# Performance work log

Hardware: AMD Instinct MI355X
Metric: run time of the kernel (lower is better)

## Reference

```python
import jax, jax.numpy as jnp
import numpy as np

B, S, D_IN, D_HID, D_LAT = 64, 1024, 256, 512, 128
GRU_DIMS = [D_LAT, 256, 128]
D_OUT = 2
EPS_BN = 1e-5
EPS_LN = 1e-5


def _lin(key, out_d, in_d):
    k1, k2 = jax.random.split(key)
    s = 1.0 / np.sqrt(in_d)
    return (jax.random.uniform(k1, (out_d, in_d), jnp.float32, -s, s),
            jax.random.uniform(k2, (out_d,), jnp.float32, -s, s))


def setup_inputs() -> dict:
    key = jax.random.key(0)
    ks = jax.random.split(key, 16)
    x = jax.random.normal(ks[0], (B, S, D_IN), jnp.float32)
    eps = jax.random.normal(ks[1], (B, S, D_LAT), jnp.float32)
    W1lv, b1lv = _lin(ks[2], D_HID, D_IN)
    W2lv, b2lv = _lin(ks[3], D_LAT, D_HID)
    Wmu, bmu = _lin(ks[4], D_LAT, D_IN)
    Wdec, bdec = _lin(ks[5], D_IN, D_LAT)
    # GRU layer 0: in=128 -> hid=256; layer 1: in=256 -> hid=128
    Wih0, bih0 = _lin(ks[6], 3 * GRU_DIMS[1], GRU_DIMS[0])
    Whh0, bhh0 = _lin(ks[7], 3 * GRU_DIMS[1], GRU_DIMS[1])
    Wih1, bih1 = _lin(ks[8], 3 * GRU_DIMS[2], GRU_DIMS[1])
    Whh1, bhh1 = _lin(ks[9], 3 * GRU_DIMS[2], GRU_DIMS[2])
    fc_W, fc_b = _lin(ks[10], D_OUT, GRU_DIMS[2])
    return dict(
        x=x, eps=eps,
        W1lv=W1lv, b1lv=b1lv, W2lv=W2lv, b2lv=b2lv, Wmu=Wmu, bmu=bmu,
        bn_g=jnp.ones((D_LAT,), jnp.float32), bn_b=jnp.zeros((D_LAT,), jnp.float32),
        bn_rm=jnp.zeros((D_LAT,), jnp.float32), bn_rv=jnp.ones((D_LAT,), jnp.float32),
        Wdec=Wdec, bdec=bdec,
        Wih0=Wih0, Whh0=Whh0, bih0=bih0, bhh0=bhh0,
        Wih1=Wih1, Whh1=Whh1, bih1=bih1, bhh1=bhh1,
        ln_g0=jnp.ones((GRU_DIMS[1],), jnp.float32), ln_b0=jnp.zeros((GRU_DIMS[1],), jnp.float32),
        ln_g1=jnp.ones((GRU_DIMS[2],), jnp.float32), ln_b1=jnp.zeros((GRU_DIMS[2],), jnp.float32),
        fc_W=fc_W, fc_b=fc_b,
    )


def _gru_cell(x, h, Wih, Whh, bih, bhh):
    gi = x @ Wih.T + bih                      # [B, 3H]
    gh = h @ Whh.T + bhh
    ir, iz, inn = jnp.split(gi, 3, axis=-1)
    hr, hz, hn = jnp.split(gh, 3, axis=-1)
    r = jax.nn.sigmoid(ir + hr)
    zg = jax.nn.sigmoid(iz + hz)
    n = jnp.tanh(inn + r * hn)
    return (1.0 - zg) * n + zg * h


def _layernorm(h, g, b):
    m = jnp.mean(h, axis=-1, keepdims=True)
    v = jnp.var(h, axis=-1, keepdims=True)
    return (h - m) * jax.lax.rsqrt(v + EPS_LN) * g + b


def reference(x, eps, W1lv, b1lv, W2lv, b2lv, Wmu, bmu, bn_g, bn_b, bn_rm, bn_rv,
              Wdec, bdec, Wih0, Whh0, bih0, bhh0, Wih1, Whh1, bih1, bhh1,
              ln_g0, ln_b0, ln_g1, ln_b1, fc_W, fc_b):
    # --- Encoder ---
    xl = jnp.log(jax.nn.softplus(x))                       # [B,S,D_IN]
    h_enc = jax.nn.relu(xl @ W1lv.T + b1lv)                # [B,S,D_HID]
    logvar = h_enc @ W2lv.T + b2lv                         # [B,S,D_LAT]
    mu = xl @ Wmu.T + bmu                                  # [B,S,D_LAT]
    # BatchNorm1d over latent channel (eval mode, running stats)
    mu = (mu - bn_rm) * jax.lax.rsqrt(bn_rv + EPS_BN) * bn_g + bn_b
    mu = jnp.clip(mu, -10.0, 10.0)
    # --- Reparameterize ---
    z = mu + eps * jnp.exp(0.5 * logvar)                   # [B,S,D_LAT]
    # --- Decoder ---
    x_recon = jnp.exp(z @ Wdec.T + bdec)                   # [B,S,D_IN]
    # --- Stacked GRUCell + LayerNorm over time ---
    batch = x.shape[0]
    h0 = jnp.zeros((batch, GRU_DIMS[1]), z.dtype)
    h1 = jnp.zeros((batch, GRU_DIMS[2]), z.dtype)

    def step(carry, z_t):
        h0, h1 = carry
        h0 = _layernorm(_gru_cell(z_t, h0, Wih0, Whh0, bih0, bhh0), ln_g0, ln_b0)
        h1 = _layernorm(_gru_cell(h0, h1, Wih1, Whh1, bih1, bhh1), ln_g1, ln_b1)
        return (h0, h1), None

    (h0, h1), _ = jax.lax.scan(step, (h0, h1), jnp.swapaxes(z, 0, 1))
    # fc head (dropout is identity in eval mode); output_series=False
    v = h1 @ fc_W.T + fc_b                                 # [B, D_OUT]
    return (v, x_recon, mu, logvar)
```

## Files before the change

### kernel.cpp

```cpp
#include <hip/hip_runtime.h>
#include <cstdint>

typedef unsigned long long u64;

#define TOKENS 65536

#define WS_XL    0ULL
#define WS_HENC  67108864ULL
#define WS_GI0   0ULL
#define WS_XBUF0 201326592ULL
#define WS_XBUF1 (201326592ULL + 131072ULL)
#define WS_MUS   (201326592ULL + 196608ULL)
#define WS_MUT   (201326592ULL + 197120ULL)
#define WS_NEED  (201326592ULL + 197632ULL)

__global__ void k_prep(const float* __restrict__ bmu, const float* __restrict__ bng,
                       const float* __restrict__ bnb, const float* __restrict__ bnrm,
                       const float* __restrict__ bnrv,
                       float* __restrict__ mus, float* __restrict__ mut)
{
    int j = threadIdx.x;
    if (j < 128) {
        float s = bng[j] / sqrtf(bnrv[j] + 1e-5f);
        mus[j] = s;
        mut[j] = bmu[j] * s + bnb[j] - bnrm[j] * s;
    }
}

__global__ void k_xl(const float* __restrict__ x, float* __restrict__ xl, int n4)
{
    int i = blockIdx.x * blockDim.x + threadIdx.x;
    if (i >= n4) return;
    float4 v = ((const float4*)x)[i];
    float4 o;
    o.x = logf(v.x > 20.f ? v.x : log1pf(expf(v.x)));
    o.y = logf(v.y > 20.f ? v.y : log1pf(expf(v.y)));
    o.z = logf(v.z > 20.f ? v.z : log1pf(expf(v.z)));
    o.w = logf(v.w > 20.f ? v.w : log1pf(expf(v.w)));
    ((float4*)xl)[i] = o;
}

template<int EPI, int AZ>
__global__ __launch_bounds__(256) void k_gemm_f32(
    const float* __restrict__ A, const float* __restrict__ W,
    const float* __restrict__ svec, const float* __restrict__ tvec,
    float* __restrict__ C, int N, int K,
    const float* __restrict__ ZMU, const float* __restrict__ ZLV, const float* __restrict__ ZEP)
{
    __shared__ float As[32][132];
    __shared__ float Ws[32][132];
    const int tid = threadIdx.x;
    const int tx = tid & 15, ty = tid >> 4;
    const int m0 = blockIdx.x * 128;
    const int n0 = blockIdx.y * 128;
    float acc[8][8];
#pragma unroll
    for (int i = 0; i < 8; ++i)
#pragma unroll
        for (int j = 0; j < 8; ++j) acc[i][j] = 0.f;

    for (int k0 = 0; k0 < K; k0 += 32) {
#pragma unroll
        for (int it = 0; it < 4; ++it) {
            int id = tid + 256 * it;
            int r = id >> 3, c4 = id & 7;
            float4 av;
            if constexpr (AZ) {
                size_t idx = (size_t)(m0 + r) * K + k0 + c4 * 4;
                float4 m4 = *(const float4*)(ZMU + idx);
                float4 l4 = *(const float4*)(ZLV + idx);
                float4 e4 = *(const float4*)(ZEP + idx);
                av.x = m4.x + e4.x * expf(0.5f * l4.x);
                av.y = m4.y + e4.y * expf(0.5f * l4.y);
                av.z = m4.z + e4.z * expf(0.5f * l4.z);
                av.w = m4.w + e4.w * expf(0.5f * l4.w);
            } else {
                av = *(const float4*)(A + (size_t)(m0 + r) * K + k0 + c4 * 4);
            }
            float4 wv = *(const float4*)(W + (size_t)(n0 + r) * K + k0 + c4 * 4);
            As[c4*4+0][r] = av.x; As[c4*4+1][r] = av.y; As[c4*4+2][r] = av.z; As[c4*4+3][r] = av.w;
            Ws[c4*4+0][r] = wv.x; Ws[c4*4+1][r] = wv.y; Ws[c4*4+2][r] = wv.z; Ws[c4*4+3][r] = wv.w;
        }
        __syncthreads();
#pragma unroll
        for (int k = 0; k < 32; ++k) {
            float4 a0 = *(const float4*)&As[k][ty*8];
            float4 a1 = *(const float4*)&As[k][ty*8+4];
            float4 w0 = *(const float4*)&Ws[k][tx*8];
            float4 w1 = *(const float4*)&Ws[k][tx*8+4];
            float ar[8] = {a0.x,a0.y,a0.z,a0.w,a1.x,a1.y,a1.z,a1.w};
            float wr[8] = {w0.x,w0.y,w0.z,w0.w,w1.x,w1.y,w1.z,w1.w};
#pragma unroll
            for (int i = 0; i < 8; ++i)
#pragma unroll
                for (int j = 0; j < 8; ++j) acc[i][j] += ar[i] * wr[j];
        }
        __syncthreads();
    }
#pragma unroll
    for (int i = 0; i < 8; ++i) {
        size_t m = (size_t)m0 + ty*8 + i;
#pragma unroll
        for (int j4 = 0; j4 < 2; ++j4) {
            float o[4];
#pragma unroll
            for (int j = 0; j < 4; ++j) {
                int col = n0 + tx*8 + j4*4 + j;
                float v = acc[i][j4*4+j];
                if (svec) v *= svec[col];
                v += tvec[col];
                if constexpr (EPI == 1) v = fmaxf(v, 0.f);
                if constexpr (EPI == 2) v = fminf(fmaxf(v, -10.f), 10.f);
                if constexpr (EPI == 3) v = expf(v);
                o[j] = v;
            }
            *(float4*)(C + m * N + n0 + tx*8 + j4*4) = *(float4*)o;
        }
    }
}

__device__ __forceinline__ void tstore(u64* p, float v, unsigned tag) {
    u64 w = ((u64)tag << 32) | (u64)__builtin_bit_cast(unsigned, v);
    __hip_atomic_store(p, w, __ATOMIC_RELAXED, __HIP_MEMORY_SCOPE_AGENT);
}
__device__ __forceinline__ float tpoll(const u64* p, unsigned tag) {
    u64 w = 0; int guard = 0;
    do {
        w = __hip_atomic_load(p, __ATOMIC_RELAXED, __HIP_MEMORY_SCOPE_AGENT);
        if ((unsigned)(w >> 32) == tag) break;
        __builtin_amdgcn_s_sleep(1);
    } while (++guard < (1 << 17));
    return __builtin_bit_cast(float, (unsigned)w);
}
__device__ __forceinline__ void rbar() {
    asm volatile("s_waitcnt lgkmcnt(0)" ::: "memory");
    __builtin_amdgcn_s_barrier();
}

__global__ __launch_bounds__(256)
__attribute__((amdgpu_waves_per_eu(1, 1)))
void k_scan0(const float* gi0, const float* wh0, const float* bhh0,
             const float* lg0, const float* lb0,
             float* h0s, u64* xbuf)
{
    const int xcd  = blockIdx.x & 7;
    const int slot = blockIdx.x >> 3;
    const int b    = xcd * 8 + (slot >> 2);
    const int q    = slot & 3;
    const int tid = threadIdx.x;
    const int lane = tid & 63;
    const int wvi  = tid >> 6;

    __shared__ float s_h[256];
    __shared__ float s_g[192];
    __shared__ float s_r1[4], s_r2[4];

    int row = 0;
    if (tid < 192)
        row = (tid < 64) ? (64*q + tid)
            : (tid < 128) ? (256 + 64*q + (tid-64))
                          : (512 + 64*q + (tid-128));
    float4 wr[64];
    float bA = 0.f;
    if (tid < 192) {
        const float4* p = (const float4*)(wh0 + (size_t)row * 256);
#pragma unroll
        for (int i = 0; i < 64; ++i) wr[i] = p[i];
        bA = bhh0[row];
    }
    const float gv = lg0[tid], bv = lb0[tid];
    s_h[tid] = 0.f;
    __syncthreads();

    const float* gbase = gi0 + (size_t)b * 1024 * 768;
    float* hb = h0s + (size_t)b * 1024 * 256;
    u64* xb = xbuf + (size_t)b * 256;

    for (int t = 0; t < 1024; ++t) {
        float gr = 0.f, gz = 0.f, gn = 0.f;
        if (tid >= 192) {
            const float* gt = gbase + (size_t)t * 768;
            int u = 64*q + (tid - 192);
            gr = gt[u]; gz = gt[256 + u]; gn = gt[512 + u];
        } else {
            float a0 = bA, a1 = 0.f, a2 = 0.f, a3 = 0.f;
            const float4* H = (const float4*)s_h;
#pragma unroll
            for (int i = 0; i < 64; ++i) {
                float4 h4 = H[i];
                a0 += wr[i].x * h4.x; a1 += wr[i].y * h4.y;
                a2 += wr[i].z * h4.z; a3 += wr[i].w * h4.w;
            }
            s_g[tid] = (a0 + a1) + (a2 + a3);
        }
        rbar();
        if (tid >= 192) {
            int g = tid - 192;
            int u = 64*q + g;
            float r  = 1.f / (1.f + expf(-(gr + s_g[g])));
            float zg = 1.f / (1.f + expf(-(gz + s_g[64 + g])));
            float nn = tanhf(gn + r * s_g[128 + g]);
            float hn = (1.f - zg) * nn + zg * s_h[u];
            tstore(&xb[u], hn, (unsigned)(t + 1));
        }
        float hn = tpoll(&xb[tid], (unsigned)(t + 1));
        float sum = hn;
#pragma unroll
        for (int o = 32; o > 0; o >>= 1) sum += __shfl_xor(sum, o);
        if (lane == 0) s_r1[wvi] = sum;
        rbar();
        float m = (s_r1[0] + s_r1[1] + s_r1[2] + s_r1[3]) * (1.f / 256.f);
        float d = hn - m;
        float ss = d * d;
#pragma unroll
        for (int o = 32; o > 0; o >>= 1) ss += __shfl_xor(ss, o);
        if (lane == 0) s_r2[wvi] = ss;
        rbar();
        float va = (s_r2[0] + s_r2[1] + s_r2[2] + s_r2[3]) * (1.f / 256.f);
        float rs = 1.f / sqrtf(va + 1e-5f);
        float hl = d * rs * gv + bv;
        s_h[tid] = hl;
        if (q == 0) hb[(size_t)t * 256 + tid] = hl;
        rbar();
    }
}

__global__ __launch_bounds__(256)
__attribute__((amdgpu_waves_per_eu(1, 1)))
void k_scan1(const float* h0s, const float* wi1, const float* wh1,
             const float* bih1, const float* bhh1,
             const float* lg1, const float* lb1,
             const float* fcW, const float* fcb,
             float* vout, u64* xbuf)
{
    const int xcd  = blockIdx.x & 7;
    const int slot = blockIdx.x >> 3;
    const int b    = xcd * 8 + (slot >> 2);
    const int q    = slot & 3;
    const int tid = threadIdx.x;
    const int lane = tid & 63;
    const int wvi  = tid >> 6;

    __shared__ float s_x[2][256];
    __shared__ float s_h[128];
    __shared__ float s_g[192];
    __shared__ float s_r1[2], s_r2[2];

    float4 wr[64];
    float bB = 0.f;
    if (tid < 96) {
        int jj = tid;
        int row = (jj < 32) ? (32*q + jj) : (jj < 64) ? (128 + 32*q + (jj-32)) : (256 + 32*q + (jj-64));
        const float4* p = (const float4*)(wi1 + (size_t)row * 256);
#pragma unroll
        for (int i = 0; i < 64; ++i) wr[i] = p[i];
        bB = bih1[row];
    } else if (tid < 192) {
        int jj = tid - 96;
        int row = (jj < 32) ? (32*q + jj) : (jj < 64) ? (128 + 32*q + (jj-32)) : (256 + 32*q + (jj-64));
        const float4* p = (const float4*)(wh1 + (size_t)row * 128);
#pragma unroll
        for (int i = 0; i < 32; ++i) wr[i] = p[i];
        bB = bhh1[row];
    }
    float gv = 0.f, bv = 0.f;
    if (tid < 128) { gv = lg1[tid]; bv = lb1[tid]; s_h[tid] = 0.f; }
    const float4* xb4 = (const float4*)(h0s + (size_t)b * 1024 * 256);
    if (tid < 64) ((float4*)s_x[0])[tid] = xb4[tid];
    __syncthreads();

    u64* xb = xbuf + (size_t)b * 128;

    for (int t = 0; t < 1024; ++t) {
        const int cur = t & 1, nxt = cur ^ 1;
        float4 st0, st1;
        const bool stg = (tid >= 224) && (t + 1 < 1024);
        if (stg) {
            int k = tid - 224;
            st0 = xb4[(size_t)(t+1) * 64 + k];
            st1 = xb4[(size_t)(t+1) * 64 + k + 32];
        }
        if (tid < 96) {
            float a0 = bB, a1 = 0.f, a2 = 0.f, a3 = 0.f;
            const float4* X = (const float4*)s_x[cur];
#pragma unroll
            for (int i = 0; i < 64; ++i) {
                float4 h4 = X[i];
                a0 += wr[i].x * h4.x; a1 += wr[i].y * h4.y;
                a2 += wr[i].z * h4.z; a3 += wr[i].w * h4.w;
            }
            s_g[tid] = (a0 + a1) + (a2 + a3);
        } else if (tid < 192) {
            float a0 = bB, a1 = 0.f, a2 = 0.f, a3 = 0.f;
            const float4* Hh = (const float4*)s_h;
#pragma unroll
            for (int i = 0; i < 32; ++i) {
                float4 h4 = Hh[i];
                a0 += wr[i].x * h4.x; a1 += wr[i].y * h4.y;
                a2 += wr[i].z * h4.z; a3 += wr[i].w * h4.w;
            }
            s_g[96 + (tid - 96)] = (a0 + a1) + (a2 + a3);
        }
        rbar();
        if (tid >= 192 && tid < 224) {
            int g = tid - 192;
            int u = 32*q + g;
            float r  = 1.f / (1.f + expf(-(s_g[g]      + s_g[96 + g])));
            float zg = 1.f / (1.f + expf(-(s_g[32 + g] + s_g[128 + g])));
            float nn = tanhf(s_g[64 + g] + r * s_g[160 + g]);
            float hn = (1.f - zg) * nn + zg * s_h[u];
            tstore(&xb[u], hn, (unsigned)(t + 1));
        } else if (stg) {
            int k = tid - 224;
            ((float4*)s_x[nxt])[k]      = st0;
            ((float4*)s_x[nxt])[k + 32] = st1;
        }
        float hn = 0.f, d = 0.f;
        if (tid < 128) {
            hn = tpoll(&xb[tid], (unsigned)(t + 1));
            float sum = hn;
#pragma unroll
            for (int o = 32; o > 0; o >>= 1) sum += __shfl_xor(sum, o);
            if (lane == 0) s_r1[wvi] = sum;
        }
        rbar();
        if (tid < 128) {
            float m = (s_r1[0] + s_r1[1]) * (1.f / 128.f);
            d = hn - m;
            float ss = d * d;
#pragma unroll
            for (int o = 32; o > 0; o >>= 1) ss += __shfl_xor(ss, o);
            if (lane == 0) s_r2[wvi] = ss;
        }
        rbar();
        if (tid < 128) {
            float va = (s_r2[0] + s_r2[1]) * (1.f / 128.f);
            float rs = 1.f / sqrtf(va + 1e-5f);
            float hl = d * rs * gv + bv;
            s_h[tid] = hl;
        }
        rbar();
    }
    float p0 = 0.f, p1 = 0.f;
    if (tid < 128) {
        float hold = s_h[tid];
        p0 = fcW[tid] * hold;
        p1 = fcW[128 + tid] * hold;
#pragma unroll
        for (int o = 32; o > 0; o >>= 1) { p0 += __shfl_xor(p0, o); p1 += __shfl_xor(p1, o); }
        if (lane == 0) { s_r1[wvi] = p0; s_r2[wvi] = p1; }
    }
    __syncthreads();
    if (tid == 0 && q == 0) {
        vout[b * 2 + 0] = s_r1[0] + s_r1[1] + fcb[0];
        vout[b * 2 + 1] = s_r2[0] + s_r2[1] + fcb[1];
    }
}

extern "C" void kernel_launch(void* const* d_in, const int* in_sizes, int n_in,
                              void* d_out, int out_size, void* d_ws, size_t ws_size,
                              hipStream_t stream)
{
    const float* x     = (const float*)d_in[0];
    const float* eps   = (const float*)d_in[1];
    const float* W1lv  = (const float*)d_in[2];
    const float* b1lv  = (const float*)d_in[3];
    const float* W2lv  = (const float*)d_in[4];
    const float* b2lv  = (const float*)d_in[5];
    const float* Wmu   = (const float*)d_in[6];
    const float* bmu   = (const float*)d_in[7];
    const float* bn_g  = (const float*)d_in[8];
    const float* bn_b  = (const float*)d_in[9];
    const float* bn_rm = (const float*)d_in[10];
    const float* bn_rv = (const float*)d_in[11];
    const float* Wdec  = (const float*)d_in[12];
    const float* bdec  = (const float*)d_in[13];
    const float* Wih0  = (const float*)d_in[14];
    const float* Whh0  = (const float*)d_in[15];
    const float* bih0  = (const float*)d_in[16];
    const float* bhh0  = (const float*)d_in[17];
    const float* Wih1  = (const float*)d_in[18];
    const float* Whh1  = (const float*)d_in[19];
    const float* bih1  = (const float*)d_in[20];
    const float* bhh1  = (const float*)d_in[21];
    const float* ln_g0 = (const float*)d_in[22];
    const float* ln_b0 = (const float*)d_in[23];
    const float* ln_g1 = (const float*)d_in[24];
    const float* ln_b1 = (const float*)d_in[25];
    const float* fc_W  = (const float*)d_in[26];
    const float* fc_b  = (const float*)d_in[27];

    float* out   = (float*)d_out;
    float* v_out = out;
    float* xrec  = out + 128;
    float* mu    = out + 128 + 16777216;
    float* lv    = out + 128 + 16777216 + 8388608;
    float* H0S   = xrec;

    if (ws_size < WS_NEED) return;
    char* ws = (char*)d_ws;
    float* XL    = (float*)(ws + WS_XL);
    float* HENC  = (float*)(ws + WS_HENC);
    float* GI0   = (float*)(ws + WS_GI0);
    u64*   XBUF0 = (u64*)(ws + WS_XBUF0);
    u64*   XBUF1 = (u64*)(ws + WS_XBUF1);
    float* MUS   = (float*)(ws + WS_MUS);
    float* MUT   = (float*)(ws + WS_MUT);

    k_prep<<<1, 128, 0, stream>>>(bmu, bn_g, bn_b, bn_rm, bn_rv, MUS, MUT);
    k_xl<<<16384, 256, 0, stream>>>(x, XL, 4194304);
    k_gemm_f32<1,0><<<dim3(512, 4), 256, 0, stream>>>(XL,   W1lv, nullptr, b1lv, HENC, 512, 256, nullptr, nullptr, nullptr);
    k_gemm_f32<0,0><<<dim3(512, 1), 256, 0, stream>>>(HENC, W2lv, nullptr, b2lv, lv,   128, 512, nullptr, nullptr, nullptr);
    k_gemm_f32<2,0><<<dim3(512, 1), 256, 0, stream>>>(XL,   Wmu,  MUS,     MUT,  mu,   128, 256, nullptr, nullptr, nullptr);
    k_gemm_f32<0,1><<<dim3(512, 6), 256, 0, stream>>>(nullptr, Wih0, nullptr, bih0, GI0, 768, 128, mu, lv, eps);
    hipMemsetAsync(XBUF0, 0, 196608, stream);
    k_scan0<<<256, 256, 0, stream>>>(GI0, Whh0, bhh0, ln_g0, ln_b0, H0S, XBUF0);
    k_scan1<<<256, 256, 0, stream>>>(H0S, Wih1, Whh1, bih1, bhh1, ln_g1, ln_b1, fc_W, fc_b, v_out, XBUF1);
    k_gemm_f32<3,1><<<dim3(512, 2), 256, 0, stream>>>(nullptr, Wdec, nullptr, bdec, xrec, 256, 128, mu, lv, eps);
}
```

Baseline: 8.001 ms.

## Add fast sc0 exchange path with parity double-buffered tags and prefetch

The per-step cross-block exchange in both GRU scan kernels now writes each tagged hidden value twice: once with a plain sc0 store/load pair and once with the agent-scope atomic. Readers poll the fast copy a bounded number of times, then fall back to the atomic path for good. Exchange buffers are double-buffered by step parity, and the GI0 / h0s input loads are prefetched one step further ahead. The aim is to cut inter-block handoff latency on the sequential critical path, at the cost of extra stores and reliance on sc0 coherence behaviour across CUs on the same XCD.

After: 9.313 ms. 1.16x slower.

```diff
diff --git a/kernel.cpp b/kernel.cpp
--- a/kernel.cpp
+++ b/kernel.cpp
@@ -8,11 +8,13 @@
 #define WS_XL    0ULL
 #define WS_HENC  67108864ULL
 #define WS_GI0   0ULL
-#define WS_XBUF0 201326592ULL
-#define WS_XBUF1 (201326592ULL + 131072ULL)
-#define WS_MUS   (201326592ULL + 196608ULL)
-#define WS_MUT   (201326592ULL + 197120ULL)
-#define WS_NEED  (201326592ULL + 197632ULL)
+#define WS_SLOW0 201326592ULL
+#define WS_SLOW1 (201326592ULL + 262144ULL)
+#define WS_FAST0 (201326592ULL + 393216ULL)
+#define WS_FAST1 (201326592ULL + 655360ULL)
+#define WS_MUS   (201326592ULL + 786432ULL)
+#define WS_MUT   (201326592ULL + 786944ULL)
+#define WS_NEED  (201326592ULL + 787456ULL)
 
 __global__ void k_prep(const float* __restrict__ bmu, const float* __restrict__ bng,
                        const float* __restrict__ bnb, const float* __restrict__ bnrm,
@@ -119,14 +121,34 @@
     }
 }
 
-__device__ __forceinline__ void tstore(u64* p, float v, unsigned tag) {
-    u64 w = ((u64)tag << 32) | (u64)__builtin_bit_cast(unsigned, v);
+__device__ __forceinline__ u64 packtag(float v, unsigned tag) {
+    return ((u64)tag << 32) | (u64)__builtin_bit_cast(unsigned, v);
+}
+__device__ __forceinline__ void tstore(u64* p, u64 w) {
     __hip_atomic_store(p, w, __ATOMIC_RELAXED, __HIP_MEMORY_SCOPE_AGENT);
 }
-__device__ __forceinline__ float tpoll(const u64* p, unsigned tag) {
+__device__ __forceinline__ void fstore(u64* p, u64 w) {
+    asm volatile("global_store_dwordx2 %0, %1, off sc0" :: "v"(p), "v"(w) : "memory");
+}
+__device__ __forceinline__ u64 fload(const u64* p) {
+    u64 w;
+    asm volatile("global_load_dwordx2 %0, %1, off sc0\n\ts_waitcnt vmcnt(0)"
+                 : "=v"(w) : "v"(p) : "memory");
+    return w;
+}
+__device__ __forceinline__ float tpoll2(const u64* fast, const u64* slow,
+                                        unsigned tag, int& slowmode) {
+    if (!slowmode) {
+        for (int k = 0; k < 24; ++k) {
+            u64 w = fload(fast);
+            if ((unsigned)(w >> 32) == tag) return __builtin_bit_cast(float, (unsigned)w);
+            __builtin_amdgcn_s_sleep(1);
+        }
+        slowmode = 1;
+    }
     u64 w = 0; int guard = 0;
     do {
-        w = __hip_atomic_load(p, __ATOMIC_RELAXED, __HIP_MEMORY_SCOPE_AGENT);
+        w = __hip_atomic_load(slow, __ATOMIC_RELAXED, __HIP_MEMORY_SCOPE_AGENT);
         if ((unsigned)(w >> 32) == tag) break;
         __builtin_amdgcn_s_sleep(1);
     } while (++guard < (1 << 17));
@@ -141,7 +163,7 @@
 __attribute__((amdgpu_waves_per_eu(1, 1)))
 void k_scan0(const float* gi0, const float* wh0, const float* bhh0,
              const float* lg0, const float* lb0,
-             float* h0s, u64* xbuf)
+             float* h0s, u64* slow, u64* fast)
 {
     const int xcd  = blockIdx.x & 7;
     const int slot = blockIdx.x >> 3;
@@ -174,14 +196,25 @@
 
     const float* gbase = gi0 + (size_t)b * 1024 * 768;
     float* hb = h0s + (size_t)b * 1024 * 256;
-    u64* xb = xbuf + (size_t)b * 256;
+    u64* sb = slow + (size_t)b * 512;
+    u64* fb = fast + (size_t)b * 512;
+    int slowmode = 0;
+
+    float pgr = 0.f, pgz = 0.f, pgn = 0.f;
+    if (tid >= 192) {
+        int u = 64*q + lane;
+        pgr = gbase[u]; pgz = gbase[256 + u]; pgn = gbase[512 + u];
+    }
 
     for (int t = 0; t < 1024; ++t) {
-        float gr = 0.f, gz = 0.f, gn = 0.f;
+        const int par = t & 1;
+        float ngr = 0.f, ngz = 0.f, ngn = 0.f;
         if (tid >= 192) {
-            const float* gt = gbase + (size_t)t * 768;
-            int u = 64*q + (tid - 192);
-            gr = gt[u]; gz = gt[256 + u]; gn = gt[512 + u];
+            if (t + 1 < 1024) {
+                const float* gt = gbase + (size_t)(t+1) * 768;
+                int u = 64*q + lane;
+                ngr = gt[u]; ngz = gt[256 + u]; ngn = gt[512 + u];
+            }
         } else {
             float a0 = bA, a1 = 0.f, a2 = 0.f, a3 = 0.f;
             const float4* H = (const float4*)s_h;
@@ -195,15 +228,18 @@
         }
         rbar();
         if (tid >= 192) {
-            int g = tid - 192;
+            int g = lane;
             int u = 64*q + g;
-            float r  = 1.f / (1.f + expf(-(gr + s_g[g])));
-            float zg = 1.f / (1.f + expf(-(gz + s_g[64 + g])));
-            float nn = tanhf(gn + r * s_g[128 + g]);
+            float r  = 1.f / (1.f + expf(-(pgr + s_g[g])));
+            float zg = 1.f / (1.f + expf(-(pgz + s_g[64 + g])));
+            float nn = tanhf(pgn + r * s_g[128 + g]);
             float hn = (1.f - zg) * nn + zg * s_h[u];
-            tstore(&xb[u], hn, (unsigned)(t + 1));
-        }
-        float hn = tpoll(&xb[tid], (unsigned)(t + 1));
+            u64 w = packtag(hn, (unsigned)(t + 1));
+            fstore(&fb[par * 256 + u], w);
+            tstore(&sb[par * 256 + u], w);
+        }
+        float hn = tpoll2(&fb[par * 256 + tid], &sb[par * 256 + tid],
+                          (unsigned)(t + 1), slowmode);
         float sum = hn;
 #pragma unroll
         for (int o = 32; o > 0; o >>= 1) sum += __shfl_xor(sum, o);
@@ -222,6 +258,7 @@
         s_h[tid] = hl;
         if (q == 0) hb[(size_t)t * 256 + tid] = hl;
         rbar();
+        pgr = ngr; pgz = ngz; pgn = ngn;
     }
 }
 
@@ -231,7 +268,7 @@
              const float* bih1, const float* bhh1,
              const float* lg1, const float* lb1,
              const float* fcW, const float* fcb,
-             float* vout, u64* xbuf)
+             float* vout, u64* slow, u64* fast)
 {
     const int xcd  = blockIdx.x & 7;
     const int slot = blockIdx.x >> 3;
@@ -267,18 +304,26 @@
     if (tid < 128) { gv = lg1[tid]; bv = lb1[tid]; s_h[tid] = 0.f; }
     const float4* xb4 = (const float4*)(h0s + (size_t)b * 1024 * 256);
     if (tid < 64) ((float4*)s_x[0])[tid] = xb4[tid];
+    float4 pp0 = {0,0,0,0}, pp1 = {0,0,0,0};
+    if (tid >= 224) {
+        int k = tid - 224;
+        pp0 = xb4[(size_t)64 + k];
+        pp1 = xb4[(size_t)64 + k + 32];
+    }
     __syncthreads();
 
-    u64* xb = xbuf + (size_t)b * 128;
+    u64* sb = slow + (size_t)b * 256;
+    u64* fb = fast + (size_t)b * 256;
+    int slowmode = 0;
 
     for (int t = 0; t < 1024; ++t) {
         const int cur = t & 1, nxt = cur ^ 1;
-        float4 st0, st1;
-        const bool stg = (tid >= 224) && (t + 1 < 1024);
-        if (stg) {
+        const int par = t & 1;
+        float4 nn0 = {0,0,0,0}, nn1 = {0,0,0,0};
+        if (tid >= 224 && t + 2 < 1024) {
             int k = tid - 224;
-            st0 = xb4[(size_t)(t+1) * 64 + k];
-            st1 = xb4[(size_t)(t+1) * 64 + k + 32];
+            nn0 = xb4[(size_t)(t+2) * 64 + k];
+            nn1 = xb4[(size_t)(t+2) * 64 + k + 32];
         }
         if (tid < 96) {
             float a0 = bB, a1 = 0.f, a2 = 0.f, a3 = 0.f;
@@ -309,15 +354,18 @@
             float zg = 1.f / (1.f + expf(-(s_g[32 + g] + s_g[128 + g])));
             float nn = tanhf(s_g[64 + g] + r * s_g[160 + g]);
             float hn = (1.f - zg) * nn + zg * s_h[u];
-            tstore(&xb[u], hn, (unsigned)(t + 1));
-        } else if (stg) {
+            u64 w = packtag(hn, (unsigned)(t + 1));
+            fstore(&fb[par * 128 + u], w);
+            tstore(&sb[par * 128 + u], w);
+        } else if (tid >= 224 && t + 1 < 1024) {
             int k = tid - 224;
-            ((float4*)s_x[nxt])[k]      = st0;
-            ((float4*)s_x[nxt])[k + 32] = st1;
+            ((float4*)s_x[nxt])[k]      = pp0;
+            ((float4*)s_x[nxt])[k + 32] = pp1;
         }
         float hn = 0.f, d = 0.f;
         if (tid < 128) {
-            hn = tpoll(&xb[tid], (unsigned)(t + 1));
+            hn = tpoll2(&fb[par * 128 + tid], &sb[par * 128 + tid],
+                        (unsigned)(t + 1), slowmode);
             float sum = hn;
 #pragma unroll
             for (int o = 32; o > 0; o >>= 1) sum += __shfl_xor(sum, o);
@@ -340,6 +388,7 @@
             s_h[tid] = hl;
         }
         rbar();
+        pp0 = nn0; pp1 = nn1;
     }
     float p0 = 0.f, p1 = 0.f;
     if (tid < 128) {
@@ -402,8 +451,10 @@
     float* XL    = (float*)(ws + WS_XL);
     float* HENC  = (float*)(ws + WS_HENC);
     float* GI0   = (float*)(ws + WS_GI0);
-    u64*   XBUF0 = (u64*)(ws + WS_XBUF0);
-    u64*   XBUF1 = (u64*)(ws + WS_XBUF1);
+    u64*   SLOW0 = (u64*)(ws + WS_SLOW0);
+    u64*   SLOW1 = (u64*)(ws + WS_SLOW1);
+    u64*   FAST0 = (u64*)(ws + WS_FAST0);
+    u64*   FAST1 = (u64*)(ws + WS_FAST1);
     float* MUS   = (float*)(ws + WS_MUS);
     float* MUT   = (float*)(ws + WS_MUT);
 
@@ -413,8 +464,8 @@
     k_gemm_f32<0,0><<<dim3(512, 1), 256, 0, stream>>>(HENC, W2lv, nullptr, b2lv, lv,   128, 512, nullptr, nullptr, nullptr);
     k_gemm_f32<2,0><<<dim3(512, 1), 256, 0, stream>>>(XL,   Wmu,  MUS,     MUT,  mu,   128, 256, nullptr, nullptr, nullptr);
     k_gemm_f32<0,1><<<dim3(512, 6), 256, 0, stream>>>(nullptr, Wih0, nullptr, bih0, GI0, 768, 128, mu, lv, eps);
-    hipMemsetAsync(XBUF0, 0, 196608, stream);
-    k_scan0<<<256, 256, 0, stream>>>(GI0, Whh0, bhh0, ln_g0, ln_b0, H0S, XBUF0);
-    k_scan1<<<256, 256, 0, stream>>>(H0S, Wih1, Whh1, bih1, bhh1, ln_g1, ln_b1, fc_W, fc_b, v_out, XBUF1);
+    hipMemsetAsync(SLOW0, 0, 786432, stream);
+    k_scan0<<<256, 256, 0, stream>>>(GI0, Whh0, bhh0, ln_g0, ln_b0, H0S, SLOW0, FAST0);
+    k_scan1<<<256, 256, 0, stream>>>(H0S, Wih1, Whh1, bih1, bhh1, ln_g1, ln_b1, fc_W, fc_b, v_out, SLOW1, FAST1);
     k_gemm_f32<3,1><<<dim3(512, 2), 256, 0, stream>>>(nullptr, Wdec, nullptr, bdec, xrec, 256, 128, mu, lv, eps);
 }
```

## Hoist GRU layer-1 input projection out of scan and drop cross-block polling

Applied to the files above, without the earlier changes.

The layer-1 input-gate projection (h0 @ Wih1) moves out of the sequential scan into a separate parallel kernel that writes gi1 to the workspace. The layer-1 scan then runs one 512-thread block per batch row, holding only the Whh1 rows in registers and prefetching gi1 two steps ahead. This removes the per-step global store/poll exchange between four blocks and shortens the serial critical path. The cost is an extra ~100MB workspace round-trip and only 64 active blocks during the scan.

After: 6.906 ms (median of 2 runs). 13.7% less time.

```diff
diff --git a/kernel.cpp b/kernel.cpp
--- a/kernel.cpp
+++ b/kernel.cpp
@@ -8,8 +8,8 @@
 #define WS_XL    0ULL
 #define WS_HENC  67108864ULL
 #define WS_GI0   0ULL
+#define WS_GI1   0ULL
 #define WS_XBUF0 201326592ULL
-#define WS_XBUF1 (201326592ULL + 131072ULL)
 #define WS_MUS   (201326592ULL + 196608ULL)
 #define WS_MUT   (201326592ULL + 197120ULL)
 #define WS_NEED  (201326592ULL + 197632ULL)
@@ -227,70 +227,109 @@
 
 __global__ __launch_bounds__(256)
 __attribute__((amdgpu_waves_per_eu(1, 1)))
-void k_scan1(const float* h0s, const float* wi1, const float* wh1,
-             const float* bih1, const float* bhh1,
-             const float* lg1, const float* lb1,
-             const float* fcW, const float* fcb,
-             float* vout, u64* xbuf)
-{
-    const int xcd  = blockIdx.x & 7;
-    const int slot = blockIdx.x >> 3;
-    const int b    = xcd * 8 + (slot >> 2);
-    const int q    = slot & 3;
+void k_gi1(const float* h0s, const float* wi1, const float* bih1, float* gi1)
+{
+    const int bx = blockIdx.x;
+    const int by = blockIdx.y;
+    const int tid = threadIdx.x;
+    __shared__ float s_x[2][4][256];
+
+    float4 wr[64];
+    float bB = 0.f;
+    const int row = by * 192 + tid;
+    if (tid < 192) {
+        const float4* p = (const float4*)(wi1 + (size_t)row * 256);
+#pragma unroll
+        for (int i = 0; i < 64; ++i) wr[i] = p[i];
+        bB = bih1[row];
+    }
+    const float4* xb4 = (const float4*)(h0s + (size_t)bx * 256 * 256);
+    if (tid >= 192) {
+        int s = tid - 192;
+#pragma unroll
+        for (int j = 0; j < 4; ++j)
+            ((float4*)s_x[0][j])[s] = xb4[(size_t)j * 64 + s];
+    }
+    __syncthreads();
+    for (int r = 0; r < 64; ++r) {
+        const int cur = r & 1;
+        float4 pf[4];
+        const bool stg = (tid >= 192) && (r + 1 < 64);
+        if (stg) {
+            int s = tid - 192;
+#pragma unroll
+            for (int j = 0; j < 4; ++j)
+                pf[j] = xb4[(size_t)((r + 1) * 4 + j) * 64 + s];
+        }
+        if (tid < 192) {
+#pragma unroll 1
+            for (int j = 0; j < 4; ++j) {
+                float a0 = bB, a1 = 0.f, a2 = 0.f, a3 = 0.f;
+                const float4* X = (const float4*)s_x[cur][j];
+#pragma unroll
+                for (int i = 0; i < 64; ++i) {
+                    float4 h4 = X[i];
+                    a0 += wr[i].x * h4.x; a1 += wr[i].y * h4.y;
+                    a2 += wr[i].z * h4.z; a3 += wr[i].w * h4.w;
+                }
+                gi1[(size_t)(bx * 256 + r * 4 + j) * 384 + row] = (a0 + a1) + (a2 + a3);
+            }
+        } else if (stg) {
+            int s = tid - 192;
+#pragma unroll
+            for (int j = 0; j < 4; ++j)
+                ((float4*)s_x[cur ^ 1][j])[s] = pf[j];
+        }
+        __syncthreads();
+    }
+}
+
+__global__ __launch_bounds__(512)
+__attribute__((amdgpu_waves_per_eu(1, 2)))
+void k_scan1(const float* gi1, const float* wh1,
+             const float* bhh1, const float* lg1, const float* lb1,
+             const float* fcW, const float* fcb, float* vout)
+{
+    const int b   = blockIdx.x;
     const int tid = threadIdx.x;
     const int lane = tid & 63;
     const int wvi  = tid >> 6;
 
-    __shared__ float s_x[2][256];
     __shared__ float s_h[128];
-    __shared__ float s_g[192];
+    __shared__ float s_g[384];
+    __shared__ float s_gi[2][384];
     __shared__ float s_r1[2], s_r2[2];
 
-    float4 wr[64];
+    float4 wr[32];
     float bB = 0.f;
-    if (tid < 96) {
-        int jj = tid;
-        int row = (jj < 32) ? (32*q + jj) : (jj < 64) ? (128 + 32*q + (jj-32)) : (256 + 32*q + (jj-64));
-        const float4* p = (const float4*)(wi1 + (size_t)row * 256);
-#pragma unroll
-        for (int i = 0; i < 64; ++i) wr[i] = p[i];
-        bB = bih1[row];
-    } else if (tid < 192) {
-        int jj = tid - 96;
-        int row = (jj < 32) ? (32*q + jj) : (jj < 64) ? (128 + 32*q + (jj-32)) : (256 + 32*q + (jj-64));
-        const float4* p = (const float4*)(wh1 + (size_t)row * 128);
+    if (tid < 384) {
+        const float4* p = (const float4*)(wh1 + (size_t)tid * 128);
 #pragma unroll
         for (int i = 0; i < 32; ++i) wr[i] = p[i];
-        bB = bhh1[row];
+        bB = bhh1[tid];
     }
     float gv = 0.f, bv = 0.f;
     if (tid < 128) { gv = lg1[tid]; bv = lb1[tid]; s_h[tid] = 0.f; }
-    const float4* xb4 = (const float4*)(h0s + (size_t)b * 1024 * 256);
-    if (tid < 64) ((float4*)s_x[0])[tid] = xb4[tid];
+
+    const float* gb = gi1 + (size_t)b * 1024 * 384;
+    float p_r = 0.f, p_z = 0.f, p_n = 0.f;
+    if (tid >= 384) {
+        int u = tid - 384;
+        s_gi[0][u] = gb[u]; s_gi[0][128 + u] = gb[128 + u]; s_gi[0][256 + u] = gb[256 + u];
+        const float* g1 = gb + 384;
+        p_r = g1[u]; p_z = g1[128 + u]; p_n = g1[256 + u];
+    }
     __syncthreads();
 
-    u64* xb = xbuf + (size_t)b * 128;
-
     for (int t = 0; t < 1024; ++t) {
-        const int cur = t & 1, nxt = cur ^ 1;
-        float4 st0, st1;
-        const bool stg = (tid >= 224) && (t + 1 < 1024);
-        if (stg) {
-            int k = tid - 224;
-            st0 = xb4[(size_t)(t+1) * 64 + k];
-            st1 = xb4[(size_t)(t+1) * 64 + k + 32];
-        }
-        if (tid < 96) {
-            float a0 = bB, a1 = 0.f, a2 = 0.f, a3 = 0.f;
-            const float4* X = (const float4*)s_x[cur];
-#pragma unroll
-            for (int i = 0; i < 64; ++i) {
-                float4 h4 = X[i];
-                a0 += wr[i].x * h4.x; a1 += wr[i].y * h4.y;
-                a2 += wr[i].z * h4.z; a3 += wr[i].w * h4.w;
-            }
-            s_g[tid] = (a0 + a1) + (a2 + a3);
-        } else if (tid < 192) {
+        const int cur = t & 1;
+        float f_r = 0.f, f_z = 0.f, f_n = 0.f;
+        if (tid >= 384 && t + 2 < 1024) {
+            const float* gt = gb + (size_t)(t + 2) * 384;
+            int u = tid - 384;
+            f_r = gt[u]; f_z = gt[128 + u]; f_n = gt[256 + u];
+        }
+        if (tid < 384) {
             float a0 = bB, a1 = 0.f, a2 = 0.f, a3 = 0.f;
             const float4* Hh = (const float4*)s_h;
 #pragma unroll
@@ -299,29 +338,22 @@
                 a0 += wr[i].x * h4.x; a1 += wr[i].y * h4.y;
                 a2 += wr[i].z * h4.z; a3 += wr[i].w * h4.w;
             }
-            s_g[96 + (tid - 96)] = (a0 + a1) + (a2 + a3);
-        }
-        rbar();
-        if (tid >= 192 && tid < 224) {
-            int g = tid - 192;
-            int u = 32*q + g;
-            float r  = 1.f / (1.f + expf(-(s_g[g]      + s_g[96 + g])));
-            float zg = 1.f / (1.f + expf(-(s_g[32 + g] + s_g[128 + g])));
-            float nn = tanhf(s_g[64 + g] + r * s_g[160 + g]);
-            float hn = (1.f - zg) * nn + zg * s_h[u];
-            tstore(&xb[u], hn, (unsigned)(t + 1));
-        } else if (stg) {
-            int k = tid - 224;
-            ((float4*)s_x[nxt])[k]      = st0;
-            ((float4*)s_x[nxt])[k + 32] = st1;
-        }
+            s_g[tid] = (a0 + a1) + (a2 + a3);
+        }
+        rbar();
         float hn = 0.f, d = 0.f;
         if (tid < 128) {
-            hn = tpoll(&xb[tid], (unsigned)(t + 1));
+            float r  = 1.f / (1.f + expf(-(s_gi[cur][tid]       + s_g[tid])));
+            float zg = 1.f / (1.f + expf(-(s_gi[cur][128 + tid] + s_g[128 + tid])));
+            float nn = tanhf(s_gi[cur][256 + tid] + r * s_g[256 + tid]);
+            hn = (1.f - zg) * nn + zg * s_h[tid];
             float sum = hn;
 #pragma unroll
             for (int o = 32; o > 0; o >>= 1) sum += __shfl_xor(sum, o);
             if (lane == 0) s_r1[wvi] = sum;
+        } else if (tid >= 384 && t + 1 < 1024) {
+            int u = tid - 384;
+            s_gi[cur ^ 1][u] = p_r; s_gi[cur ^ 1][128 + u] = p_z; s_gi[cur ^ 1][256 + u] = p_n;
         }
         rbar();
         if (tid < 128) {
@@ -336,10 +368,10 @@
         if (tid < 128) {
             float va = (s_r2[0] + s_r2[1]) * (1.f / 128.f);
             float rs = 1.f / sqrtf(va + 1e-5f);
-            float hl = d * rs * gv + bv;
-            s_h[tid] = hl;
-        }
-        rbar();
+            s_h[tid] = d * rs * gv + bv;
+        }
+        rbar();
+        p_r = f_r; p_z = f_z; p_n = f_n;
     }
     float p0 = 0.f, p1 = 0.f;
     if (tid < 128) {
@@ -351,7 +383,7 @@
         if (lane == 0) { s_r1[wvi] = p0; s_r2[wvi] = p1; }
     }
     __syncthreads();
-    if (tid == 0 && q == 0) {
+    if (tid == 0) {
         vout[b * 2 + 0] = s_r1[0] + s_r1[1] + fcb[0];
         vout[b * 2 + 1] = s_r2[0] + s_r2[1] + fcb[1];
     }
@@ -402,8 +434,8 @@
     float* XL    = (float*)(ws + WS_XL);
     float* HENC  = (float*)(ws + WS_HENC);
     float* GI0   = (float*)(ws + WS_GI0);
+    float* GI1   = (float*)(ws + WS_GI1);
     u64*   XBUF0 = (u64*)(ws + WS_XBUF0);
-    u64*   XBUF1 = (u64*)(ws + WS_XBUF1);
     float* MUS   = (float*)(ws + WS_MUS);
     float* MUT   = (float*)(ws + WS_MUT);
 
@@ -413,8 +445,9 @@
     k_gemm_f32<0,0><<<dim3(512, 1), 256, 0, stream>>>(HENC, W2lv, nullptr, b2lv, lv,   128, 512, nullptr, nullptr, nullptr);
     k_gemm_f32<2,0><<<dim3(512, 1), 256, 0, stream>>>(XL,   Wmu,  MUS,     MUT,  mu,   128, 256, nullptr, nullptr, nullptr);
     k_gemm_f32<0,1><<<dim3(512, 6), 256, 0, stream>>>(nullptr, Wih0, nullptr, bih0, GI0, 768, 128, mu, lv, eps);
-    hipMemsetAsync(XBUF0, 0, 196608, stream);
+    hipMemsetAsync(XBUF0, 0, 131072, stream);
     k_scan0<<<256, 256, 0, stream>>>(GI0, Whh0, bhh0, ln_g0, ln_b0, H0S, XBUF0);
-    k_scan1<<<256, 256, 0, stream>>>(H0S, Wih1, Whh1, bih1, bhh1, ln_g1, ln_b1, fc_W, fc_b, v_out, XBUF1);
+    k_gi1<<<dim3(256, 2), 256, 0, stream>>>(H0S, Wih1, bih1, GI1);
     k_gemm_f32<3,1><<<dim3(512, 2), 256, 0, stream>>>(nullptr, Wdec, nullptr, bdec, xrec, 256, 128, mu, lv, eps);
-}
+    k_scan1<<<64, 512, 0, stream>>>(GI1, Whh1, bhh1, ln_g1, ln_b1, fc_W, fc_b, v_out);
+}
```
